# Performance work log

Measured on AMD Instinct MI355X. Metric: run time of the kernel, lower is better.

## Reference

```python
import jax, jax.numpy as jnp
import numpy as np

EPS = 1e-6
INPUT_SIZE = 64
NUM_LEAVES = INPUT_SIZE
NUM_LAYERS = NUM_LEAVES - 1
BATCH = 262144
SINKHORN_ITERS = 20


def _clip01(v):
    return jnp.clip(v, EPS, 1.0 - EPS)


def _F_base(x, y, a, w0, w1):
    # Branches of F for a in [0.5, 2] (the non-recursive region), selected branchlessly.
    x = _clip01(x)
    y = _clip01(y)
    lin = w0 * x + w1 * y
    p = jnp.sqrt(3.0 / jnp.maximum(2.0 - a, EPS)) - 1.0
    g = (x ** (2.0 * w0) * y ** (2.0 * w1)) ** p
    rule0 = jnp.where((jnp.abs(x - 1.0) < EPS) & (jnp.abs(y - 1.0) < EPS), 1.0, 0.0)
    return jnp.where(
        jnp.abs(a - 2.0) < EPS, rule0,
        jnp.where(a >= 0.75, g,
                  jnp.where(a > 0.5, (3.0 - 4.0 * a) * lin + (4.0 * a - 2.0) * g, lin)))


def _F(x, y, a, w0, w1):
    # Full generalized_gcd F with the single-level De Morgan reflection for a < 0.5.
    x = _clip01(x)
    y = _clip01(y)
    hi = _F_base(x, y, a, w0, w1)
    a_ref = jnp.clip(1.0 - a, -1.0 + EPS, 2.0 - EPS)
    lo = 1.0 - _F_base(1.0 - x, 1.0 - y, a_ref, w0, w1)
    lin = w0 * x + w1 * y
    return jnp.where(jnp.abs(a - 0.5) < EPS, lin, jnp.where(a < 0.5, lo, hi))


def _sinkhorn(logits, n_iter=SINKHORN_ITERS):
    # Log-space Sinkhorn normalization -> (approximately) doubly-stochastic P.
    l = logits
    for _ in range(n_iter):
        l = l - jax.nn.logsumexp(l, axis=1, keepdims=True)
        l = l - jax.nn.logsumexp(l, axis=0, keepdims=True)
    return jnp.exp(l)


def setup_inputs() -> dict:
    key = jax.random.key(0)
    k1, k2, k3, k4 = jax.random.split(key, 4)
    x = jax.random.uniform(k1, (BATCH, INPUT_SIZE), dtype=jnp.float32)
    logits = jax.random.normal(k2, (INPUT_SIZE, NUM_LEAVES), dtype=jnp.float32)
    weights = jax.random.uniform(k3, (NUM_LAYERS,), dtype=jnp.float32)
    biases = jax.random.uniform(k4, (NUM_LAYERS,), dtype=jnp.float32)
    return {"x": x, "logits": logits, "weights": weights, "biases": biases}


def reference(x, logits, weights, biases):
    P = _sinkhorn(logits)                 # [INPUT_SIZE, NUM_LEAVES], columns sum to 1
    leaves = (x @ P).T                    # [NUM_LEAVES, BATCH]

    def step(carry, inp):
        leaf, w, b = inp
        nres = _F(carry, leaf, b, w, 1.0 - w)
        nres = jnp.where(jnp.isnan(nres), b, nres)  # NaN fallback to bias, as in torch forward
        return nres, None

    # Left-leaning tree: state_0 = leaf_0; state_i = F(state_{i-1}, leaf_i, b, w, 1-w)
    final, _ = jax.lax.scan(step, leaves[0], (leaves[1:], weights, biases))
    return final[:, None]                 # [BATCH, 1]
```

## Files before the change

### kernel.cpp

```cpp
#include <hip/hip_runtime.h>
#include <hip/hip_bf16.h>
#include <math.h>

#define EPS 1e-6f
#define NLAYERS 63
#define SINK_ITERS 20
#define LOG2E 1.4426950408889634f

typedef __attribute__((ext_vector_type(8))) short bf16x8;
typedef __attribute__((ext_vector_type(4))) float f32x4;
typedef __attribute__((ext_vector_type(4))) unsigned int ui32x4;

__device__ __forceinline__ float fast_log2(float v) {
#if __has_builtin(__builtin_amdgcn_logf)
  return __builtin_amdgcn_logf(v);
#else
  return log2f(v);
#endif
}
__device__ __forceinline__ float fast_exp2(float v) {
#if __has_builtin(__builtin_amdgcn_exp2f)
  return __builtin_amdgcn_exp2f(v);
#else
  return exp2f(v);
#endif
}

__device__ __forceinline__ unsigned int f2bf(float f) {
  unsigned int u = __float_as_uint(f);
  return (u + 0x7FFFu + ((u >> 16) & 1u)) >> 16;
}

__device__ __forceinline__ unsigned int cvt_pk_bf16(float lo, float hi) {
  unsigned int r;
  asm("v_cvt_pk_bf16_f32 %0, %1, %2" : "=v"(r) : "v"(lo), "v"(hi));
  return r;
}
__device__ __forceinline__ bf16x8 pack8(float4 a, float4 b) {
  ui32x4 u;
  u[0] = cvt_pk_bf16(a.x, a.y);
  u[1] = cvt_pk_bf16(a.z, a.w);
  u[2] = cvt_pk_bf16(b.x, b.y);
  u[3] = cvt_pk_bf16(b.z, b.w);
  return __builtin_bit_cast(bf16x8, u);
}


template<int HALF>
__device__ __forceinline__ void do_gemm(const bf16x8 (&Bf)[2][4],
                                        const bf16x8 (&Af)[4][2],
                                        float* Lv, int w, int q, int c) {
  #pragma unroll
  for (int rt = 0; rt < 4; ++rt) {
    #pragma unroll
    for (int lt = 0; lt < 2; ++lt) {
      f32x4 acc = {0.f, 0.f, 0.f, 0.f};
      acc = __builtin_amdgcn_mfma_f32_16x16x32_bf16(Bf[0][(HALF << 1) + lt], Af[rt][0], acc, 0, 0, 0);
      acc = __builtin_amdgcn_mfma_f32_16x16x32_bf16(Bf[1][(HALF << 1) + lt], Af[rt][1], acc, 0, 0, 0);
      const int row  = (w << 6) + (rt << 4) + c;
      const int nloc = (lt << 4) + (q << 2);
      *(f32x4*)&Lv[row * 36 + nloc] = acc;
    }
  }
}

template<int L0>
__device__ __forceinline__ void do_chunk(const float* Lrow,
                                         const float* Lcst, float& r) {
  constexpr int loc = L0 & 31;
  f32x4 lf0 = *(const f32x4*)&Lrow[loc];
  f32x4 lf1 = *(const f32x4*)&Lrow[loc + 4];
  float lf[8] = {lf0[0], lf0[1], lf0[2], lf0[3], lf1[0], lf1[1], lf1[2], lf1[3]};

  float ylin[8], ylg[8];
  #pragma unroll
  for (int k = 0; k < 8; ++k) {
    if (L0 + k >= 1) {
      float4 p0 = *(const float4*)&Lcst[(L0 + k - 1) * 8];
      float off = fmaf(-0.5f, p0.x, 0.5f);
      float yy  = fminf(fmaxf(lf[k], EPS), 1.0f - EPS);
      float yr  = fmaf(p0.x, yy, off);
      float ly  = fast_log2(yr);
      ylg[k]  = fmaf(p0.y, ly, p0.z);
      ylin[k] = p0.w * yr;
    }
  }

  #pragma unroll
  for (int k = 0; k < 8; ++k) {
    if (L0 + k >= 1) {
      float4 p1 = *(const float4*)&Lcst[(L0 + k - 1) * 8 + 4];
      float cr = fminf(fmaxf(r, EPS), 1.0f - EPS);
      float xr = fmaf(p1.x, cr, p1.y);
      float lx = fast_log2(xr);
      float g  = fast_exp2(fmaf(p1.z, lx, ylg[k]));
      r = fmaf(p1.w, xr, ylin[k]) + g;
    } else {
      r = lf[0];
    }
  }
}

__device__ __forceinline__ void run_pass(const bf16x8 (&Bf)[2][4],
                                         const bf16x8 (&Af)[4][2],
                                         float* Lv, const float* Lcst,
                                         float* __restrict__ out,
                                         size_t rowbase, int tid,
                                         int w, int q, int c) {
  const float* Lrow = &Lv[tid * 36];
  float r = 0.f;

  do_gemm<0>(Bf, Af, Lv, w, q, c);
  do_chunk<0>(Lrow, Lcst, r);
  do_chunk<8>(Lrow, Lcst, r);
  do_chunk<16>(Lrow, Lcst, r);
  do_chunk<24>(Lrow, Lcst, r);

  do_gemm<1>(Bf, Af, Lv, w, q, c);
  do_chunk<32>(Lrow, Lcst, r);
  do_chunk<40>(Lrow, Lcst, r);
  do_chunk<48>(Lrow, Lcst, r);
  do_chunk<56>(Lrow, Lcst, r);

  const float sgnL = Lcst[62 * 8];
  out[rowbase + tid] = fmaf(sgnL, r, fmaf(-0.5f, sgnL, 0.5f));
}

__global__ __launch_bounds__(256) void fused_kernel(
    const float* __restrict__ x,
    const float* __restrict__ logits,
    const float* __restrict__ weights,
    const float* __restrict__ biases,
    float* __restrict__ out) {
  __shared__ float T[64 * 65];
  __shared__ float Uv[64];
  __shared__ float Vv[64];
  __shared__ float part[4][64];
  __shared__ float Lcst[NLAYERS * 8];
  __shared__ float Lv[256 * 36];

  const int tid = threadIdx.x;
  const int w = tid >> 6, l = tid & 63;
  const int q = l >> 4, c = l & 15;
  const size_t rowbase0 = (size_t)blockIdx.x << 9;

  bf16x8 Af[4][2];
  {
    const float* rp0 = x + (rowbase0 + (w << 6) + c) * 64 + (q << 3);
    float4 t0[4], t1[4];
    #define LOADROW(dst, i) do {                                   \
      const float* rp = rp0 + ((i) << 4) * 64;                     \
      (dst)[0] = *(const float4*)(rp);                             \
      (dst)[1] = *(const float4*)(rp + 4);                         \
      (dst)[2] = *(const float4*)(rp + 32);                        \
      (dst)[3] = *(const float4*)(rp + 36);                        \
    } while (0)
    LOADROW(t0, 0);
    LOADROW(t1, 1);
    Af[0][0] = pack8(t0[0], t0[1]); Af[0][1] = pack8(t0[2], t0[3]);
    LOADROW(t0, 2);
    Af[1][0] = pack8(t1[0], t1[1]); Af[1][1] = pack8(t1[2], t1[3]);
    LOADROW(t1, 3);
    Af[2][0] = pack8(t0[0], t0[1]); Af[2][1] = pack8(t0[2], t0[3]);
    Af[3][0] = pack8(t1[0], t1[1]); Af[3][1] = pack8(t1[2], t1[3]);
    #undef LOADROW
  }

  if (tid < NLAYERS) {
    float w0 = weights[tid];
    float w1 = 1.0f - w0;
    float a  = biases[tid];
    float sgn, e0, e1, cw0, cw1, lcg;
    if (fabsf(a - 0.5f) < EPS) {
      sgn = 1.f; e0 = 0.f; e1 = 0.f; cw0 = w0; cw1 = w1; lcg = -1.0e30f;
    } else {
      float ae;
      if (a < 0.5f) { sgn = -1.f; ae = fminf(fmaxf(1.0f - a, -1.0f + EPS), 2.0f - EPS); }
      else          { sgn =  1.f; ae = a; }
      float pp = sqrtf(3.0f / fmaxf(2.0f - ae, EPS)) - 1.0f;
      float cl, cg;
      if (ae >= 0.75f) { cl = 0.0f;            cg = 1.0f; }
      else             { cl = 3.0f - 4.0f*ae;  cg = 4.0f*ae - 2.0f; }
      e0  = 2.0f * w0 * pp;
      e1  = 2.0f * w1 * pp;
      cw0 = cl * w0;
      cw1 = cl * w1;
      lcg = (cg > 0.f) ? log2f(cg) : -1.0e30f;
    }
    float sgnp = 1.f;
    if (tid > 0) {
      float ap = biases[tid - 1];
      sgnp = (fabsf(ap - 0.5f) < EPS) ? 1.f : (ap < 0.5f ? -1.f : 1.f);
    }
    float Sc = sgn * sgnp;
    float Oc = 0.5f - 0.5f * Sc;
    float* Lr = Lcst + tid * 8;
    Lr[0] = sgn; Lr[1] = e1; Lr[2] = lcg; Lr[3] = cw1;
    Lr[4] = Sc;  Lr[5] = Oc; Lr[6] = e0;  Lr[7] = cw0;
  }

  float K_part[16], KT_part[16];
  {
    const float4* lr = (const float4*)(logits + (l << 6) + (w << 4));
    #pragma unroll
    for (int i = 0; i < 4; ++i) {
      float4 t = lr[i];
      K_part[4*i+0] = fast_exp2(t.x * LOG2E);
      K_part[4*i+1] = fast_exp2(t.y * LOG2E);
      K_part[4*i+2] = fast_exp2(t.z * LOG2E);
      K_part[4*i+3] = fast_exp2(t.w * LOG2E);
    }
  }
  #pragma unroll
  for (int i = 0; i < 16; ++i) T[l * 65 + (w << 4) + i] = K_part[i];
  if (tid < 64) Vv[tid] = 1.0f;
  __syncthreads();
  #pragma unroll
  for (int i = 0; i < 16; ++i) KT_part[i] = T[((w << 4) + i) * 65 + l];

  for (int it = 0; it < SINK_ITERS; ++it) {
    float p0 = 0.f, p1 = 0.f, p2 = 0.f, p3 = 0.f;
    #pragma unroll
    for (int i = 0; i < 4; ++i) {
      p0 = fmaf(K_part[4*i+0], Vv[(w << 4) + 4*i+0], p0);
      p1 = fmaf(K_part[4*i+1], Vv[(w << 4) + 4*i+1], p1);
      p2 = fmaf(K_part[4*i+2], Vv[(w << 4) + 4*i+2], p2);
      p3 = fmaf(K_part[4*i+3], Vv[(w << 4) + 4*i+3], p3);
    }
    part[w][l] = (p0 + p1) + (p2 + p3);
    __syncthreads();
    if (tid < 64) {
      float s = (part[0][tid] + part[1][tid]) + (part[2][tid] + part[3][tid]);
      Uv[tid] = 1.0f / s;
    }
    __syncthreads();
    float q0 = 0.f, q1 = 0.f, q2 = 0.f, q3 = 0.f;
    #pragma unroll
    for (int i = 0; i < 4; ++i) {
      q0 = fmaf(KT_part[4*i+0], Uv[(w << 4) + 4*i+0], q0);
      q1 = fmaf(KT_part[4*i+1], Uv[(w << 4) + 4*i+1], q1);
      q2 = fmaf(KT_part[4*i+2], Uv[(w << 4) + 4*i+2], q2);
      q3 = fmaf(KT_part[4*i+3], Uv[(w << 4) + 4*i+3], q3);
    }
    part[w][l] = (q0 + q1) + (q2 + q3);
    __syncthreads();
    if (tid < 64) {
      float s = (part[0][tid] + part[1][tid]) + (part[2][tid] + part[3][tid]);
      Vv[tid] = 1.0f / s;
    }
    __syncthreads();
  }

  {
    const float ul = Uv[l];
    #pragma unroll
    for (int i = 0; i < 16; ++i)
      T[l * 65 + (w << 4) + i] = ul * K_part[i] * Vv[(w << 4) + i];
  }
  __syncthreads();

  bf16x8 Bf[2][4];
  #pragma unroll
  for (int s = 0; s < 2; ++s)
    #pragma unroll
    for (int t = 0; t < 4; ++t) {
      ui32x4 u;
      #pragma unroll
      for (int jj = 0; jj < 4; ++jj) {
        unsigned int lo = f2bf(T[(s*32 + (q << 3) + 2*jj    ) * 65 + t*16 + c]);
        unsigned int hi = f2bf(T[(s*32 + (q << 3) + 2*jj + 1) * 65 + t*16 + c]);
        u[jj] = lo | (hi << 16);
      }
      Bf[s][t] = __builtin_bit_cast(bf16x8, u);
    }

  run_pass(Bf, Af, Lv, Lcst, out, rowbase0, tid, w, q, c);

  {
    bf16x8 Af2[4][2];
    const float* rp0 = x + (rowbase0 + 256 + (w << 6) + c) * 64 + (q << 3);
    float4 t0[4], t1[4];
    #define LOADROW2(dst, i) do {                                  \
      const float* rp = rp0 + ((i) << 4) * 64;                     \
      (dst)[0] = *(const float4*)(rp);                             \
      (dst)[1] = *(const float4*)(rp + 4);                         \
      (dst)[2] = *(const float4*)(rp + 32);                        \
      (dst)[3] = *(const float4*)(rp + 36);                        \
    } while (0)
    LOADROW2(t0, 0);
    LOADROW2(t1, 1);
    Af2[0][0] = pack8(t0[0], t0[1]); Af2[0][1] = pack8(t0[2], t0[3]);
    LOADROW2(t0, 2);
    Af2[1][0] = pack8(t1[0], t1[1]); Af2[1][1] = pack8(t1[2], t1[3]);
    LOADROW2(t1, 3);
    Af2[2][0] = pack8(t0[0], t0[1]); Af2[2][1] = pack8(t0[2], t0[3]);
    Af2[3][0] = pack8(t1[0], t1[1]); Af2[3][1] = pack8(t1[2], t1[3]);
    #undef LOADROW2
    run_pass(Bf, Af2, Lv, Lcst, out, rowbase0 + 256, tid, w, q, c);
  }
}

extern "C" void kernel_launch(void* const* d_in, const int* in_sizes, int n_in,
                              void* d_out, int out_size, void* d_ws, size_t ws_size,
                              hipStream_t stream) {
  const float* x       = (const float*)d_in[0];
  const float* logits  = (const float*)d_in[1];
  const float* weights = (const float*)d_in[2];
  const float* biases  = (const float*)d_in[3];
  float* out = (float*)d_out;

  const int batch = out_size;
  hipLaunchKernelGGL(fused_kernel, dim3(batch / 512), dim3(256), 0, stream,
                     x, logits, weights, biases, out);
}
```

Baseline: 139.2 us.

## Process one 256-row tile per block and alias shared memory for occupancy

Each block now handles 256 rows instead of two back-to-back 512-row passes, which doubles the grid size. The Lv, T and other shared arrays are merged into one aliased buffer to shrink LDS per block, and launch bounds request 4 blocks per CU. The aim is higher occupancy, so the serial 63-layer chain and the global loads of different blocks can overlap. In exchange, the 20-iteration Sinkhorn preamble is now recomputed twice as many times in total, and the aliasing of T with Lv requires the added barrier.

```diff
diff --git a/kernel.cpp b/kernel.cpp
--- a/kernel.cpp
+++ b/kernel.cpp
@@ -101,52 +101,28 @@
   }
 }
 
-__device__ __forceinline__ void run_pass(const bf16x8 (&Bf)[2][4],
-                                         const bf16x8 (&Af)[4][2],
-                                         float* Lv, const float* Lcst,
-                                         float* __restrict__ out,
-                                         size_t rowbase, int tid,
-                                         int w, int q, int c) {
-  const float* Lrow = &Lv[tid * 36];
-  float r = 0.f;
-
-  do_gemm<0>(Bf, Af, Lv, w, q, c);
-  do_chunk<0>(Lrow, Lcst, r);
-  do_chunk<8>(Lrow, Lcst, r);
-  do_chunk<16>(Lrow, Lcst, r);
-  do_chunk<24>(Lrow, Lcst, r);
-
-  do_gemm<1>(Bf, Af, Lv, w, q, c);
-  do_chunk<32>(Lrow, Lcst, r);
-  do_chunk<40>(Lrow, Lcst, r);
-  do_chunk<48>(Lrow, Lcst, r);
-  do_chunk<56>(Lrow, Lcst, r);
-
-  const float sgnL = Lcst[62 * 8];
-  out[rowbase + tid] = fmaf(sgnL, r, fmaf(-0.5f, sgnL, 0.5f));
-}
-
-__global__ __launch_bounds__(256) void fused_kernel(
+__global__ __launch_bounds__(256, 4) void fused_kernel(
     const float* __restrict__ x,
     const float* __restrict__ logits,
     const float* __restrict__ weights,
     const float* __restrict__ biases,
     float* __restrict__ out) {
-  __shared__ float T[64 * 65];
-  __shared__ float Uv[64];
-  __shared__ float Vv[64];
-  __shared__ float part[4][64];
-  __shared__ float Lcst[NLAYERS * 8];
-  __shared__ float Lv[256 * 36];
+  __shared__ float SMEM[10104];
+  float* Lv   = SMEM;
+  float* T    = SMEM;
+  float* Lcst = SMEM + 9216;
+  float* part = SMEM + 9720;
+  float* Uv   = SMEM + 9976;
+  float* Vv   = SMEM + 10040;
 
   const int tid = threadIdx.x;
   const int w = tid >> 6, l = tid & 63;
   const int q = l >> 4, c = l & 15;
-  const size_t rowbase0 = (size_t)blockIdx.x << 9;
+  const size_t rowbase = (size_t)blockIdx.x << 8;
 
   bf16x8 Af[4][2];
   {
-    const float* rp0 = x + (rowbase0 + (w << 6) + c) * 64 + (q << 3);
+    const float* rp0 = x + (rowbase + (w << 6) + c) * 64 + (q << 3);
     float4 t0[4], t1[4];
     #define LOADROW(dst, i) do {                                   \
       const float* rp = rp0 + ((i) << 4) * 64;                     \
@@ -227,10 +203,10 @@
       p2 = fmaf(K_part[4*i+2], Vv[(w << 4) + 4*i+2], p2);
       p3 = fmaf(K_part[4*i+3], Vv[(w << 4) + 4*i+3], p3);
     }
-    part[w][l] = (p0 + p1) + (p2 + p3);
+    part[(w << 6) + l] = (p0 + p1) + (p2 + p3);
     __syncthreads();
     if (tid < 64) {
-      float s = (part[0][tid] + part[1][tid]) + (part[2][tid] + part[3][tid]);
+      float s = (part[tid] + part[64 + tid]) + (part[128 + tid] + part[192 + tid]);
       Uv[tid] = 1.0f / s;
     }
     __syncthreads();
@@ -242,10 +218,10 @@
       q2 = fmaf(KT_part[4*i+2], Uv[(w << 4) + 4*i+2], q2);
       q3 = fmaf(KT_part[4*i+3], Uv[(w << 4) + 4*i+3], q3);
     }
-    part[w][l] = (q0 + q1) + (q2 + q3);
+    part[(w << 6) + l] = (q0 + q1) + (q2 + q3);
     __syncthreads();
     if (tid < 64) {
-      float s = (part[0][tid] + part[1][tid]) + (part[2][tid] + part[3][tid]);
+      float s = (part[tid] + part[64 + tid]) + (part[128 + tid] + part[192 + tid]);
       Vv[tid] = 1.0f / s;
     }
     __syncthreads();
@@ -273,31 +249,25 @@
       }
       Bf[s][t] = __builtin_bit_cast(bf16x8, u);
     }
-
-  run_pass(Bf, Af, Lv, Lcst, out, rowbase0, tid, w, q, c);
-
-  {
-    bf16x8 Af2[4][2];
-    const float* rp0 = x + (rowbase0 + 256 + (w << 6) + c) * 64 + (q << 3);
-    float4 t0[4], t1[4];
-    #define LOADROW2(dst, i) do {                                  \
-      const float* rp = rp0 + ((i) << 4) * 64;                     \
-      (dst)[0] = *(const float4*)(rp);                             \
-      (dst)[1] = *(const float4*)(rp + 4);                         \
-      (dst)[2] = *(const float4*)(rp + 32);                        \
-      (dst)[3] = *(const float4*)(rp + 36);                        \
-    } while (0)
-    LOADROW2(t0, 0);
-    LOADROW2(t1, 1);
-    Af2[0][0] = pack8(t0[0], t0[1]); Af2[0][1] = pack8(t0[2], t0[3]);
-    LOADROW2(t0, 2);
-    Af2[1][0] = pack8(t1[0], t1[1]); Af2[1][1] = pack8(t1[2], t1[3]);
-    LOADROW2(t1, 3);
-    Af2[2][0] = pack8(t0[0], t0[1]); Af2[2][1] = pack8(t0[2], t0[3]);
-    Af2[3][0] = pack8(t1[0], t1[1]); Af2[3][1] = pack8(t1[2], t1[3]);
-    #undef LOADROW2
-    run_pass(Bf, Af2, Lv, Lcst, out, rowbase0 + 256, tid, w, q, c);
-  }
+  __syncthreads();
+
+  const float* Lrow = &Lv[tid * 36];
+  float r = 0.f;
+
+  do_gemm<0>(Bf, Af, Lv, w, q, c);
+  do_chunk<0>(Lrow, Lcst, r);
+  do_chunk<8>(Lrow, Lcst, r);
+  do_chunk<16>(Lrow, Lcst, r);
+  do_chunk<24>(Lrow, Lcst, r);
+
+  do_gemm<1>(Bf, Af, Lv, w, q, c);
+  do_chunk<32>(Lrow, Lcst, r);
+  do_chunk<40>(Lrow, Lcst, r);
+  do_chunk<48>(Lrow, Lcst, r);
+  do_chunk<56>(Lrow, Lcst, r);
+
+  const float sgnL = Lcst[62 * 8];
+  out[rowbase + tid] = fmaf(sgnL, r, fmaf(-0.5f, sgnL, 0.5f));
 }
 
 extern "C" void kernel_launch(void* const* d_in, const int* in_sizes, int n_in,
@@ -310,6 +280,6 @@
   float* out = (float*)d_out;
 
   const int batch = out_size;
-  hipLaunchKernelGGL(fused_kernel, dim3(batch / 512), dim3(256), 0, stream,
+  hipLaunchKernelGGL(fused_kernel, dim3(batch / 256), dim3(256), 0, stream,
                      x, logits, weights, biases, out);
 }
```

New measurement: 119.9 us. 1.16x faster.
